# Performance work log

Measured on AMD Instinct MI355X. Metric: run time of the kernel, lower is better.

The kernel has to match this reference:

```python
import jax, jax.numpy as jnp
import numpy as np

N = 50000
E = 800000
IN_C = 128
HID_C = 128
OUT_C = 128
N_CLS = 40


def setup_inputs() -> dict:
    key = jax.random.key(0)
    ks = jax.random.split(key, 12)
    x = jax.random.normal(ks[0], (N, IN_C), dtype=jnp.float32)
    edge_index = jax.random.randint(ks[1], (2, E), 0, N, dtype=jnp.int64)
    s = 1.0 / np.sqrt(IN_C)
    W_l1 = jax.random.uniform(ks[2], (IN_C, HID_C), jnp.float32, -s, s)
    W_r1 = jax.random.uniform(ks[3], (IN_C, HID_C), jnp.float32, -s, s)
    b1 = jax.random.uniform(ks[4], (HID_C,), jnp.float32, -s, s)
    s2 = 1.0 / np.sqrt(HID_C)
    W_l2 = jax.random.uniform(ks[5], (HID_C, OUT_C), jnp.float32, -s2, s2)
    W_r2 = jax.random.uniform(ks[6], (HID_C, OUT_C), jnp.float32, -s2, s2)
    b2 = jax.random.uniform(ks[7], (OUT_C,), jnp.float32, -s2, s2)
    s3 = 1.0 / np.sqrt(OUT_C)
    W_c = jax.random.uniform(ks[8], (OUT_C, N_CLS), jnp.float32, -s3, s3)
    b_c = jax.random.uniform(ks[9], (N_CLS,), jnp.float32, -s3, s3)
    return {"x": x, "edge_index": edge_index, "W_l1": W_l1, "W_r1": W_r1,
            "b1": b1, "W_l2": W_l2, "W_r2": W_r2, "b2": b2,
            "W_c": W_c, "b_c": b_c}


def _mean_aggregate(x, src, dst, deg_inv):
    # gather source node features over edges, scatter-mean to dst nodes
    msg = x[src]  # [E, C]
    agg = jax.ops.segment_sum(msg, dst, num_segments=N)  # [N, C]
    return agg * deg_inv[:, None]


def _sage_conv(x, src, dst, deg_inv, W_l, W_r, b):
    # PyG SAGEConv (mean aggr): out = agg @ W_l + x @ W_r + b
    agg = _mean_aggregate(x, src, dst, deg_inv)
    return agg @ W_l + x @ W_r + b


def reference(x, edge_index, W_l1, W_r1, b1, W_l2, W_r2, b2, W_c, b_c):
    src, dst = edge_index[0], edge_index[1]
    deg = jax.ops.segment_sum(jnp.ones((E,), jnp.float32), dst, num_segments=N)
    deg_inv = jnp.where(deg > 0, 1.0 / jnp.maximum(deg, 1.0), 0.0)
    h = jax.nn.relu(_sage_conv(x, src, dst, deg_inv, W_l1, W_r1, b1))
    h = jax.nn.relu(_sage_conv(h, src, dst, deg_inv, W_l2, W_r2, b2))
    return h @ W_c + b_c
```

## Files before the change

### kernel.cpp

```cpp
#include <hip/hip_runtime.h>

#define N_NODES 50000
#define N_EDGES 800000
#define C 128
#define NCLS 40
#define KB 98
#define BCAP 9216

typedef short bf16x8 __attribute__((ext_vector_type(8)));
typedef float f32x4 __attribute__((ext_vector_type(4)));
typedef unsigned short ushort_t;

__device__ __forceinline__ unsigned short f32_to_bf16(float f) {
    union { float f; unsigned u; } c; c.f = f;
    unsigned r = (c.u + 0x7FFFu + ((c.u >> 16) & 1u)) >> 16;
    return (unsigned short)r;
}
__device__ __forceinline__ float bf_lo(unsigned u) {
    union { unsigned u; float f; } c; c.u = u << 16; return c.f;
}
__device__ __forceinline__ float bf_hi(unsigned u) {
    union { unsigned u; float f; } c; c.u = u & 0xffff0000u; return c.f;
}
__device__ __forceinline__ unsigned pack_bf16(float lo, float hi) {
    return (unsigned)f32_to_bf16(lo) | ((unsigned)f32_to_bf16(hi) << 16);
}

__global__ __launch_bounds__(256)
void convert_all(const float* __restrict__ Wl1, const float* __restrict__ Wr1,
                 const float* __restrict__ Wl2, const float* __restrict__ Wr2,
                 const float* __restrict__ Wc,  const float* __restrict__ x,
                 ushort_t* __restrict__ Wbf1, ushort_t* __restrict__ Wbf2,
                 ushort_t* __restrict__ Wcb,  ushort_t* __restrict__ xb) {
    int b = blockIdx.x;
    int tid = threadIdx.x;
    if (b < 256) {
        const float* Wl = (b < 128) ? Wl1 : Wl2;
        const float* Wr = (b < 128) ? Wr1 : Wr2;
        ushort_t* Bpre  = (b < 128) ? Wbf1 : Wbf2;
        int idx = (b & 127) * 256 + tid;
        int n = idx >> 8;
        int k = idx & 255;
        float v = (k < 128) ? Wl[k * 128 + n] : Wr[(k - 128) * 128 + n];
        Bpre[n * 256 + k] = f32_to_bf16(v);
    } else if (b < 280) {
        int idx = (b - 256) * 256 + tid;
        if (idx < 48 * 128) {
            int n = idx >> 7;
            int k = idx & 127;
            float v = (n < NCLS) ? Wc[k * NCLS + n] : 0.f;
            Wcb[idx] = f32_to_bf16(v);
        }
    } else {
        int idx = (b - 280) * 256 + tid;
        const float4 v0 = *(const float4*)&x[idx * 8];
        const float4 v1 = *(const float4*)&x[idx * 8 + 4];
        uint4 o;
        o.x = pack_bf16(v0.x, v0.y);
        o.y = pack_bf16(v0.z, v0.w);
        o.z = pack_bf16(v1.x, v1.y);
        o.w = pack_bf16(v1.z, v1.w);
        ((uint4*)xb)[idx] = o;
    }
}

__global__ __launch_bounds__(256)
void bin_kernel(const int* __restrict__ src, const int* __restrict__ dst,
                int* __restrict__ bucket_cnt, unsigned* __restrict__ bucket_data) {
    __shared__ int lh[KB];
    int tid = threadIdx.x;
    int e0 = blockIdx.x * 4096;
    if (tid < KB) lh[tid] = 0;
    __syncthreads();
#pragma unroll
    for (int j = 0; j < 16; ++j) {
        int e = e0 + j * 256 + tid;
        if (e < N_EDGES) atomicAdd(&lh[dst[e] >> 9], 1);
    }
    __syncthreads();
    if (tid < KB) lh[tid] = atomicAdd(&bucket_cnt[tid], lh[tid]);
    __syncthreads();
#pragma unroll
    for (int j = 0; j < 16; ++j) {
        int e = e0 + j * 256 + tid;
        if (e < N_EDGES) {
            int d = dst[e];
            int b = d >> 9;
            int pos = atomicAdd(&lh[b], 1);
            if (pos < BCAP)
                bucket_data[b * BCAP + pos] = (unsigned)src[e] | ((unsigned)(d & 511) << 16);
        }
    }
}

__global__ __launch_bounds__(256)
void build_kernel(const int* __restrict__ bucket_cnt, const unsigned* __restrict__ bucket_data,
                  int* __restrict__ row_ptr, ushort_t* __restrict__ csr16,
                  int* __restrict__ perm) {
    __shared__ int wt[4];
    __shared__ int wt2[4];
    __shared__ int sbases[128];
    __shared__ int hist[512];
    __shared__ int loff[512];
    __shared__ int dhist[64];
    __shared__ ushort_t lcsr[BCAP];
    int tid = threadIdx.x;
    int b = blockIdx.x;
    int n0 = b << 9;
    int nb = min(512, N_NODES - n0);

    int v = 0, x = 0;
    if (tid < 128) {
        v = (tid < KB) ? bucket_cnt[tid] : 0;
        x = v;
#pragma unroll
        for (int off = 1; off < 64; off <<= 1) {
            int t = __shfl_up(x, off, 64);
            if ((tid & 63) >= off) x += t;
        }
        if ((tid & 63) == 63) wt[tid >> 6] = x;
    }
    hist[tid] = 0; hist[tid + 256] = 0;
    __syncthreads();
    if (tid < 128) sbases[tid] = x - v + ((tid >= 64) ? wt[0] : 0);
    __syncthreads();
    int base = sbases[b];
    int ecnt = min(bucket_cnt[b], BCAP);

    for (int i = tid; i < ecnt; i += 256)
        atomicAdd(&hist[bucket_data[b * BCAP + i] >> 16], 1);
    __syncthreads();

    int h0 = hist[2 * tid], h1 = hist[2 * tid + 1];
    int s = h0 + h1;
    int y = s;
#pragma unroll
    for (int off = 1; off < 64; off <<= 1) {
        int t = __shfl_up(y, off, 64);
        if ((tid & 63) >= off) y += t;
    }
    if ((tid & 63) == 63) wt2[tid >> 6] = y;
    __syncthreads();
    int add = 0;
    for (int j = 0; j < (tid >> 6); ++j) add += wt2[j];
    int ex = y + add - s;
    loff[2 * tid] = ex;
    loff[2 * tid + 1] = ex + h0;
    __syncthreads();

    for (int n = tid; n < nb; n += 256) row_ptr[n0 + n] = base + loff[n];
    if (b == KB - 1 && tid == 0) row_ptr[N_NODES] = N_EDGES;
    __syncthreads();

    for (int i = tid; i < ecnt; i += 256) {
        unsigned e = bucket_data[b * BCAP + i];
        int pos = atomicAdd(&loff[e >> 16], 1);
        lcsr[pos] = (ushort_t)(e & 0xFFFFu);
    }
    __syncthreads();
    for (int i = tid; i < ecnt; i += 256) csr16[base + i] = lcsr[i];

    if (tid < 64) dhist[tid] = 0;
    for (int p = tid; p < 512; p += 256) perm[(b << 9) + p] = -1;
    __syncthreads();
    int na = 2 * tid, nbb = 2 * tid + 1;
    int c0 = min(h0, 63), c1 = min(h1, 63);
    if (na < nb)  atomicAdd(&dhist[c0], 1);
    if (nbb < nb) atomicAdd(&dhist[c1], 1);
    __syncthreads();
    if (tid < 64) {
        int v2 = dhist[tid];
        int xs = v2;
#pragma unroll
        for (int off = 1; off < 64; off <<= 1) {
            int t = __shfl_up(xs, off, 64);
            if (tid >= off) xs += t;
        }
        dhist[tid] = xs - v2;
    }
    __syncthreads();
    if (na < nb)  { int pos = atomicAdd(&dhist[c0], 1); perm[(b << 9) + pos] = n0 + na; }
    if (nbb < nb) { int pos = atomicAdd(&dhist[c1], 1); perm[(b << 9) + pos] = n0 + nbb; }
}

#define ALD 136
template<int CLS>
__global__ __launch_bounds__(256)
void fused_layer(const ushort_t* __restrict__ feat,
                 const int* __restrict__ row_ptr,
                 const ushort_t* __restrict__ csr16,
                 const int* __restrict__ perm,
                 const ushort_t* __restrict__ Bpre,
                 const float* __restrict__ bias,
                 ushort_t* __restrict__ hout,
                 const ushort_t* __restrict__ Wcb,
                 const float* __restrict__ bc,
                 float* __restrict__ out) {
    __shared__ ushort_t aggL[64 * ALD];
    __shared__ ushort_t stg[64 * 40 + 128 * 40];
    __shared__ int tperm[64];
    ushort_t* AsX = stg;
    ushort_t* BsP = stg + 64 * 40;
    ushort_t* eidx = stg;
    const int tid = threadIdx.x;
    const int r0 = blockIdx.x * 64;
    const int w = tid >> 6, lane = tid & 63, m = lane & 15, quad = lane >> 4;
    const int q = tid & 15;
    const int g = tid >> 4;

    if (tid < 64) tperm[tid] = perm[r0 + tid];
    __syncthreads();

    for (int p = 0; p < 4; ++p) {
        int nl = p * 16 + g;
        int node = tperm[nl];
        int beg = 0, end = 0;
        if (node >= 0) { beg = row_ptr[node]; end = row_ptr[node + 1]; }
        int dl = end - beg; if (dl > 64) dl = 64;
        for (int j = q; j < dl; j += 16) eidx[nl * 64 + j] = csr16[beg + j];
    }
    __syncthreads();

    const uint4* fb = (const uint4*)feat;
    for (int p = 0; p < 4; ++p) {
        int nl = p * 16 + g;
        int node = tperm[nl];
        int beg = 0, end = 0;
        if (node >= 0) { beg = row_ptr[node]; end = row_ptr[node + 1]; }
        int deg = end - beg;
        int dl = deg > 64 ? 64 : deg;
        float a0[8], a1[8], a2[8], a3[8];
#pragma unroll
        for (int j = 0; j < 8; ++j) { a0[j] = 0.f; a1[j] = 0.f; a2[j] = 0.f; a3[j] = 0.f; }
        int i = 0;
        for (; i + 4 <= dl; i += 4) {
            ushort4 s4 = *(const ushort4*)&eidx[nl * 64 + i];
            uint4 v0 = fb[(int)s4.x * 16 + q];
            uint4 v1 = fb[(int)s4.y * 16 + q];
            uint4 v2 = fb[(int)s4.z * 16 + q];
            uint4 v3 = fb[(int)s4.w * 16 + q];
            a0[0] += bf_lo(v0.x); a0[1] += bf_hi(v0.x); a0[2] += bf_lo(v0.y); a0[3] += bf_hi(v0.y);
            a0[4] += bf_lo(v0.z); a0[5] += bf_hi(v0.z); a0[6] += bf_lo(v0.w); a0[7] += bf_hi(v0.w);
            a1[0] += bf_lo(v1.x); a1[1] += bf_hi(v1.x); a1[2] += bf_lo(v1.y); a1[3] += bf_hi(v1.y);
            a1[4] += bf_lo(v1.z); a1[5] += bf_hi(v1.z); a1[6] += bf_lo(v1.w); a1[7] += bf_hi(v1.w);
            a2[0] += bf_lo(v2.x); a2[1] += bf_hi(v2.x); a2[2] += bf_lo(v2.y); a2[3] += bf_hi(v2.y);
            a2[4] += bf_lo(v2.z); a2[5] += bf_hi(v2.z); a2[6] += bf_lo(v2.w); a2[7] += bf_hi(v2.w);
            a3[0] += bf_lo(v3.x); a3[1] += bf_hi(v3.x); a3[2] += bf_lo(v3.y); a3[3] += bf_hi(v3.y);
            a3[4] += bf_lo(v3.z); a3[5] += bf_hi(v3.z); a3[6] += bf_lo(v3.w); a3[7] += bf_hi(v3.w);
        }
        int rem = dl - i;
        if (rem > 0) {
            int s0 = eidx[nl * 64 + i];
            int s1 = eidx[nl * 64 + i + (rem > 1 ? 1 : 0)];
            int s2 = eidx[nl * 64 + i + (rem > 2 ? 2 : 0)];
            uint4 v0 = fb[s0 * 16 + q];
            uint4 v1 = fb[s1 * 16 + q];
            uint4 v2 = fb[s2 * 16 + q];
            float m1 = rem > 1 ? 1.f : 0.f;
            float m2 = rem > 2 ? 1.f : 0.f;
            a0[0] += bf_lo(v0.x); a0[1] += bf_hi(v0.x); a0[2] += bf_lo(v0.y); a0[3] += bf_hi(v0.y);
            a0[4] += bf_lo(v0.z); a0[5] += bf_hi(v0.z); a0[6] += bf_lo(v0.w); a0[7] += bf_hi(v0.w);
            a1[0] += m1 * bf_lo(v1.x); a1[1] += m1 * bf_hi(v1.x); a1[2] += m1 * bf_lo(v1.y); a1[3] += m1 * bf_hi(v1.y);
            a1[4] += m1 * bf_lo(v1.z); a1[5] += m1 * bf_hi(v1.z); a1[6] += m1 * bf_lo(v1.w); a1[7] += m1 * bf_hi(v1.w);
            a2[0] += m2 * bf_lo(v2.x); a2[1] += m2 * bf_hi(v2.x); a2[2] += m2 * bf_lo(v2.y); a2[3] += m2 * bf_hi(v2.y);
            a2[4] += m2 * bf_lo(v2.z); a2[5] += m2 * bf_hi(v2.z); a2[6] += m2 * bf_lo(v2.w); a2[7] += m2 * bf_hi(v2.w);
        }
        for (int j2 = 64; j2 < deg; ++j2) {
            int s0 = csr16[beg + j2];
            uint4 v0 = fb[s0 * 16 + q];
            a0[0] += bf_lo(v0.x); a0[1] += bf_hi(v0.x); a0[2] += bf_lo(v0.y); a0[3] += bf_hi(v0.y);
            a0[4] += bf_lo(v0.z); a0[5] += bf_hi(v0.z); a0[6] += bf_lo(v0.w); a0[7] += bf_hi(v0.w);
        }
        float di = deg > 0 ? 1.f / (float)deg : 0.f;
        float r[8];
#pragma unroll
        for (int j = 0; j < 8; ++j) r[j] = (a0[j] + a1[j] + a2[j] + a3[j]) * di;
        uint4 o;
        o.x = pack_bf16(r[0], r[1]);
        o.y = pack_bf16(r[2], r[3]);
        o.z = pack_bf16(r[4], r[5]);
        o.w = pack_bf16(r[6], r[7]);
        *(uint4*)&aggL[nl * ALD + q * 8] = o;
    }
    __syncthreads();

    f32x4 acc[8];
#pragma unroll
    for (int t = 0; t < 8; ++t) acc[t] = (f32x4){0.f, 0.f, 0.f, 0.f};

    for (int kc = 0; kc < 8; ++kc) {
        if (kc) __syncthreads();
        if (kc >= 4) {
            int row = tid >> 2;
            int kq = tid & 3;
            int nd = tperm[row]; if (nd < 0) nd = 0;
            uint4 v = *(const uint4*)&feat[nd * C + (kc & 3) * 32 + kq * 8];
            *(uint4*)&AsX[row * 40 + kq * 8] = v;
        }
#pragma unroll
        for (int i = 0; i < 2; ++i) {
            int slot = tid + i * 256;
            int n = slot >> 2;
            int qq = slot & 3;
            *(uint4*)&BsP[n * 40 + qq * 8] = *(const uint4*)&Bpre[n * 256 + kc * 32 + qq * 8];
        }
        __syncthreads();
        bf16x8 af = (kc < 4)
            ? *(const bf16x8*)&aggL[(w * 16 + m) * ALD + kc * 32 + quad * 8]
            : *(const bf16x8*)&AsX[(w * 16 + m) * 40 + quad * 8];
#pragma unroll
        for (int t = 0; t < 8; ++t) {
            bf16x8 bf = *(const bf16x8*)&BsP[(t * 16 + m) * 40 + quad * 8];
            acc[t] = __builtin_amdgcn_mfma_f32_16x16x32_bf16(af, bf, acc[t], 0, 0, 0);
        }
    }

    int prow[4];
#pragma unroll
    for (int reg = 0; reg < 4; ++reg) prow[reg] = tperm[w * 16 + quad * 4 + reg];

    if (CLS == 0) {
#pragma unroll
        for (int t = 0; t < 8; ++t) {
            int colv = t * 16 + m;
            float bv = bias[colv];
#pragma unroll
            for (int reg = 0; reg < 4; ++reg) {
                int rg = prow[reg];
                if (rg >= 0) {
                    float vv = fmaxf(acc[t][reg] + bv, 0.f);
                    hout[rg * C + colv] = f32_to_bf16(vv);
                }
            }
        }
    } else {
        __syncthreads();
#pragma unroll
        for (int t = 0; t < 8; ++t) {
            int colv = t * 16 + m;
            float bv = bias[colv];
#pragma unroll
            for (int reg = 0; reg < 4; ++reg) {
                int rl = w * 16 + quad * 4 + reg;
                float vv = fmaxf(acc[t][reg] + bv, 0.f);
                aggL[rl * ALD + colv] = f32_to_bf16(vv);
            }
        }
#pragma unroll
        for (int i = 0; i < 3; ++i) {
            int slot = tid + i * 256;
            int n = slot >> 4, kq = slot & 15;
            uint4 vv = *(const uint4*)&Wcb[n * C + kq * 8];
            *(uint4*)&stg[(kq >> 2) * (48 * 40) + n * 40 + (kq & 3) * 8] = vv;
        }
        __syncthreads();
        f32x4 acc2[3];
#pragma unroll
        for (int t = 0; t < 3; ++t) acc2[t] = (f32x4){0.f, 0.f, 0.f, 0.f};
#pragma unroll
        for (int kc = 0; kc < 4; ++kc) {
            bf16x8 af = *(const bf16x8*)&aggL[(w * 16 + m) * ALD + kc * 32 + quad * 8];
#pragma unroll
            for (int t = 0; t < 3; ++t) {
                bf16x8 bf = *(const bf16x8*)&stg[kc * (48 * 40) + (t * 16 + m) * 40 + quad * 8];
                acc2[t] = __builtin_amdgcn_mfma_f32_16x16x32_bf16(af, bf, acc2[t], 0, 0, 0);
            }
        }
#pragma unroll
        for (int t = 0; t < 3; ++t) {
            int col = t * 16 + m;
            if (col < NCLS) {
                float bvv = bc[col];
#pragma unroll
                for (int reg = 0; reg < 4; ++reg) {
                    int rg = prow[reg];
                    if (rg >= 0) out[rg * NCLS + col] = acc2[t][reg] + bvv;
                }
            }
        }
    }
}

extern "C" void kernel_launch(void* const* d_in, const int* in_sizes, int n_in,
                              void* d_out, int out_size, void* d_ws, size_t ws_size,
                              hipStream_t stream) {
    const float* x   = (const float*)d_in[0];
    const int*   ei  = (const int*)d_in[1];
    const float* Wl1 = (const float*)d_in[2];
    const float* Wr1 = (const float*)d_in[3];
    const float* b1  = (const float*)d_in[4];
    const float* Wl2 = (const float*)d_in[5];
    const float* Wr2 = (const float*)d_in[6];
    const float* b2  = (const float*)d_in[7];
    const float* Wc  = (const float*)d_in[8];
    const float* bc  = (const float*)d_in[9];
    const int* srcI = ei;
    const int* dstI = ei + N_EDGES;
    float* out = (float*)d_out;

    ushort_t* xb   = (ushort_t*)d_ws;
    ushort_t* h1b  = xb + (size_t)N_NODES * C;
    ushort_t* Wbf1 = h1b + (size_t)N_NODES * C;
    ushort_t* Wbf2 = Wbf1 + 32768;
    ushort_t* Wcb  = Wbf2 + 32768;
    ushort_t* csr16 = Wcb + 6144;
    int* bucket_cnt = (int*)(csr16 + N_EDGES);
    int* row_ptr    = bucket_cnt + 128;
    unsigned* bucket_data = (unsigned*)(row_ptr + N_NODES + 1);
    int* perm = (int*)(bucket_data + (size_t)KB * BCAP);

    convert_all<<<280 + (N_NODES * C / 8 + 255) / 256, 256, 0, stream>>>(
        Wl1, Wr1, Wl2, Wr2, Wc, x, Wbf1, Wbf2, Wcb, xb);

    hipMemsetAsync(bucket_cnt, 0, 128 * sizeof(int), stream);
    bin_kernel<<<(N_EDGES + 4095) / 4096, 256, 0, stream>>>(srcI, dstI, bucket_cnt, bucket_data);
    build_kernel<<<KB, 256, 0, stream>>>(bucket_cnt, bucket_data, row_ptr, csr16, perm);

    fused_layer<0><<<KB * 8, 256, 0, stream>>>(
        xb, row_ptr, csr16, perm, Wbf1, b1, h1b, nullptr, nullptr, nullptr);

    fused_layer<1><<<KB * 8, 256, 0, stream>>>(
        h1b, row_ptr, csr16, perm, Wbf2, b2, nullptr, Wcb, bc, out);
}
```

Measured before the change: 216.8 us.

## Split fused gather+GEMM layer into separate gather and dense GEMM kernels

Each layer's fused aggregate-then-GEMM kernel is unfused into a gather kernel and a GEMM kernel. The gather kernel handles 16 nodes per block, reads edge indices straight from global memory with one-step software prefetch, and writes the mean-aggregated features to a new workspace buffer. The GEMM kernel then tiles contiguous rows in natural order and no longer needs the perm indirection. This aims to cut per-block imbalance and LDS/sync overhead in the fused kernel. In exchange it adds an extra round trip of the aggregated features through global memory and two more kernel launches.

New measurement: 224.0 us. +3.3%, slower.

```diff
diff --git a/kernel.cpp b/kernel.cpp
--- a/kernel.cpp
+++ b/kernel.cpp
@@ -183,106 +183,98 @@
     if (nbb < nb) { int pos = atomicAdd(&dhist[c1], 1); perm[(b << 9) + pos] = n0 + nbb; }
 }
 
+__global__ __launch_bounds__(256)
+void gather_kernel(const ushort_t* __restrict__ feat,
+                   const int* __restrict__ row_ptr,
+                   const ushort_t* __restrict__ csr16,
+                   const int* __restrict__ perm,
+                   ushort_t* __restrict__ agg) {
+    const int tid = threadIdx.x;
+    const int q = tid & 15;
+    const int g = tid >> 4;
+    int slot = blockIdx.x * 16 + g;
+    int node = perm[slot];
+    if (node < 0) return;
+    int beg = row_ptr[node], end = row_ptr[node + 1];
+    int deg = end - beg;
+    const uint4* fb = (const uint4*)feat;
+
+    float a0[8], a1[8], a2[8], a3[8];
+#pragma unroll
+    for (int j = 0; j < 8; ++j) { a0[j] = 0.f; a1[j] = 0.f; a2[j] = 0.f; a3[j] = 0.f; }
+
+    int nquad = deg >> 2;
+    int sx0 = 0, sx1 = 0, sx2 = 0, sx3 = 0;
+    if (nquad > 0) {
+        sx0 = csr16[beg]; sx1 = csr16[beg + 1]; sx2 = csr16[beg + 2]; sx3 = csr16[beg + 3];
+    }
+    for (int qd = 0; qd < nquad; ++qd) {
+        int s0 = sx0, s1 = sx1, s2 = sx2, s3 = sx3;
+        uint4 v0 = fb[s0 * 16 + q];
+        uint4 v1 = fb[s1 * 16 + q];
+        uint4 v2 = fb[s2 * 16 + q];
+        uint4 v3 = fb[s3 * 16 + q];
+        if (qd + 1 < nquad) {
+            int bs = beg + (qd + 1) * 4;
+            sx0 = csr16[bs]; sx1 = csr16[bs + 1]; sx2 = csr16[bs + 2]; sx3 = csr16[bs + 3];
+        }
+        a0[0] += bf_lo(v0.x); a0[1] += bf_hi(v0.x); a0[2] += bf_lo(v0.y); a0[3] += bf_hi(v0.y);
+        a0[4] += bf_lo(v0.z); a0[5] += bf_hi(v0.z); a0[6] += bf_lo(v0.w); a0[7] += bf_hi(v0.w);
+        a1[0] += bf_lo(v1.x); a1[1] += bf_hi(v1.x); a1[2] += bf_lo(v1.y); a1[3] += bf_hi(v1.y);
+        a1[4] += bf_lo(v1.z); a1[5] += bf_hi(v1.z); a1[6] += bf_lo(v1.w); a1[7] += bf_hi(v1.w);
+        a2[0] += bf_lo(v2.x); a2[1] += bf_hi(v2.x); a2[2] += bf_lo(v2.y); a2[3] += bf_hi(v2.y);
+        a2[4] += bf_lo(v2.z); a2[5] += bf_hi(v2.z); a2[6] += bf_lo(v2.w); a2[7] += bf_hi(v2.w);
+        a3[0] += bf_lo(v3.x); a3[1] += bf_hi(v3.x); a3[2] += bf_lo(v3.y); a3[3] += bf_hi(v3.y);
+        a3[4] += bf_lo(v3.z); a3[5] += bf_hi(v3.z); a3[6] += bf_lo(v3.w); a3[7] += bf_hi(v3.w);
+    }
+    int i0 = beg + nquad * 4;
+    int rem = end - i0;
+    if (rem > 0) {
+        int s0 = csr16[i0];
+        int s1 = csr16[i0 + (rem > 1 ? 1 : 0)];
+        int s2 = csr16[i0 + (rem > 2 ? 2 : 0)];
+        uint4 v0 = fb[s0 * 16 + q];
+        uint4 v1 = fb[s1 * 16 + q];
+        uint4 v2 = fb[s2 * 16 + q];
+        float m1 = rem > 1 ? 1.f : 0.f;
+        float m2 = rem > 2 ? 1.f : 0.f;
+        a0[0] += bf_lo(v0.x); a0[1] += bf_hi(v0.x); a0[2] += bf_lo(v0.y); a0[3] += bf_hi(v0.y);
+        a0[4] += bf_lo(v0.z); a0[5] += bf_hi(v0.z); a0[6] += bf_lo(v0.w); a0[7] += bf_hi(v0.w);
+        a1[0] += m1 * bf_lo(v1.x); a1[1] += m1 * bf_hi(v1.x); a1[2] += m1 * bf_lo(v1.y); a1[3] += m1 * bf_hi(v1.y);
+        a1[4] += m1 * bf_lo(v1.z); a1[5] += m1 * bf_hi(v1.z); a1[6] += m1 * bf_lo(v1.w); a1[7] += m1 * bf_hi(v1.w);
+        a2[0] += m2 * bf_lo(v2.x); a2[1] += m2 * bf_hi(v2.x); a2[2] += m2 * bf_lo(v2.y); a2[3] += m2 * bf_hi(v2.y);
+        a2[4] += m2 * bf_lo(v2.z); a2[5] += m2 * bf_hi(v2.z); a2[6] += m2 * bf_lo(v2.w); a2[7] += m2 * bf_hi(v2.w);
+    }
+    float di = deg > 0 ? 1.f / (float)deg : 0.f;
+    float r[8];
+#pragma unroll
+    for (int j = 0; j < 8; ++j) r[j] = (a0[j] + a1[j] + a2[j] + a3[j]) * di;
+    uint4 o;
+    o.x = pack_bf16(r[0], r[1]);
+    o.y = pack_bf16(r[2], r[3]);
+    o.z = pack_bf16(r[4], r[5]);
+    o.w = pack_bf16(r[6], r[7]);
+    *(uint4*)&agg[node * C + q * 8] = o;
+}
+
 #define ALD 136
 template<int CLS>
 __global__ __launch_bounds__(256)
-void fused_layer(const ushort_t* __restrict__ feat,
-                 const int* __restrict__ row_ptr,
-                 const ushort_t* __restrict__ csr16,
-                 const int* __restrict__ perm,
-                 const ushort_t* __restrict__ Bpre,
-                 const float* __restrict__ bias,
-                 ushort_t* __restrict__ hout,
-                 const ushort_t* __restrict__ Wcb,
-                 const float* __restrict__ bc,
-                 float* __restrict__ out) {
-    __shared__ ushort_t aggL[64 * ALD];
+void gemm_layer(const ushort_t* __restrict__ agg,
+                const ushort_t* __restrict__ feat,
+                const ushort_t* __restrict__ Bpre,
+                const float* __restrict__ bias,
+                ushort_t* __restrict__ hout,
+                const ushort_t* __restrict__ Wcb,
+                const float* __restrict__ bc,
+                float* __restrict__ out) {
     __shared__ ushort_t stg[64 * 40 + 128 * 40];
-    __shared__ int tperm[64];
-    ushort_t* AsX = stg;
-    ushort_t* BsP = stg + 64 * 40;
-    ushort_t* eidx = stg;
+    __shared__ ushort_t h2L[CLS ? 64 * ALD : 4];
+    ushort_t* As = stg;
+    ushort_t* Bs = stg + 64 * 40;
     const int tid = threadIdx.x;
     const int r0 = blockIdx.x * 64;
     const int w = tid >> 6, lane = tid & 63, m = lane & 15, quad = lane >> 4;
-    const int q = tid & 15;
-    const int g = tid >> 4;
-
-    if (tid < 64) tperm[tid] = perm[r0 + tid];
-    __syncthreads();
-
-    for (int p = 0; p < 4; ++p) {
-        int nl = p * 16 + g;
-        int node = tperm[nl];
-        int beg = 0, end = 0;
-        if (node >= 0) { beg = row_ptr[node]; end = row_ptr[node + 1]; }
-        int dl = end - beg; if (dl > 64) dl = 64;
-        for (int j = q; j < dl; j += 16) eidx[nl * 64 + j] = csr16[beg + j];
-    }
-    __syncthreads();
-
-    const uint4* fb = (const uint4*)feat;
-    for (int p = 0; p < 4; ++p) {
-        int nl = p * 16 + g;
-        int node = tperm[nl];
-        int beg = 0, end = 0;
-        if (node >= 0) { beg = row_ptr[node]; end = row_ptr[node + 1]; }
-        int deg = end - beg;
-        int dl = deg > 64 ? 64 : deg;
-        float a0[8], a1[8], a2[8], a3[8];
-#pragma unroll
-        for (int j = 0; j < 8; ++j) { a0[j] = 0.f; a1[j] = 0.f; a2[j] = 0.f; a3[j] = 0.f; }
-        int i = 0;
-        for (; i + 4 <= dl; i += 4) {
-            ushort4 s4 = *(const ushort4*)&eidx[nl * 64 + i];
-            uint4 v0 = fb[(int)s4.x * 16 + q];
-            uint4 v1 = fb[(int)s4.y * 16 + q];
-            uint4 v2 = fb[(int)s4.z * 16 + q];
-            uint4 v3 = fb[(int)s4.w * 16 + q];
-            a0[0] += bf_lo(v0.x); a0[1] += bf_hi(v0.x); a0[2] += bf_lo(v0.y); a0[3] += bf_hi(v0.y);
-            a0[4] += bf_lo(v0.z); a0[5] += bf_hi(v0.z); a0[6] += bf_lo(v0.w); a0[7] += bf_hi(v0.w);
-            a1[0] += bf_lo(v1.x); a1[1] += bf_hi(v1.x); a1[2] += bf_lo(v1.y); a1[3] += bf_hi(v1.y);
-            a1[4] += bf_lo(v1.z); a1[5] += bf_hi(v1.z); a1[6] += bf_lo(v1.w); a1[7] += bf_hi(v1.w);
-            a2[0] += bf_lo(v2.x); a2[1] += bf_hi(v2.x); a2[2] += bf_lo(v2.y); a2[3] += bf_hi(v2.y);
-            a2[4] += bf_lo(v2.z); a2[5] += bf_hi(v2.z); a2[6] += bf_lo(v2.w); a2[7] += bf_hi(v2.w);
-            a3[0] += bf_lo(v3.x); a3[1] += bf_hi(v3.x); a3[2] += bf_lo(v3.y); a3[3] += bf_hi(v3.y);
-            a3[4] += bf_lo(v3.z); a3[5] += bf_hi(v3.z); a3[6] += bf_lo(v3.w); a3[7] += bf_hi(v3.w);
-        }
-        int rem = dl - i;
-        if (rem > 0) {
-            int s0 = eidx[nl * 64 + i];
-            int s1 = eidx[nl * 64 + i + (rem > 1 ? 1 : 0)];
-            int s2 = eidx[nl * 64 + i + (rem > 2 ? 2 : 0)];
-            uint4 v0 = fb[s0 * 16 + q];
-            uint4 v1 = fb[s1 * 16 + q];
-            uint4 v2 = fb[s2 * 16 + q];
-            float m1 = rem > 1 ? 1.f : 0.f;
-            float m2 = rem > 2 ? 1.f : 0.f;
-            a0[0] += bf_lo(v0.x); a0[1] += bf_hi(v0.x); a0[2] += bf_lo(v0.y); a0[3] += bf_hi(v0.y);
-            a0[4] += bf_lo(v0.z); a0[5] += bf_hi(v0.z); a0[6] += bf_lo(v0.w); a0[7] += bf_hi(v0.w);
-            a1[0] += m1 * bf_lo(v1.x); a1[1] += m1 * bf_hi(v1.x); a1[2] += m1 * bf_lo(v1.y); a1[3] += m1 * bf_hi(v1.y);
-            a1[4] += m1 * bf_lo(v1.z); a1[5] += m1 * bf_hi(v1.z); a1[6] += m1 * bf_lo(v1.w); a1[7] += m1 * bf_hi(v1.w);
-            a2[0] += m2 * bf_lo(v2.x); a2[1] += m2 * bf_hi(v2.x); a2[2] += m2 * bf_lo(v2.y); a2[3] += m2 * bf_hi(v2.y);
-            a2[4] += m2 * bf_lo(v2.z); a2[5] += m2 * bf_hi(v2.z); a2[6] += m2 * bf_lo(v2.w); a2[7] += m2 * bf_hi(v2.w);
-        }
-        for (int j2 = 64; j2 < deg; ++j2) {
-            int s0 = csr16[beg + j2];
-            uint4 v0 = fb[s0 * 16 + q];
-            a0[0] += bf_lo(v0.x); a0[1] += bf_hi(v0.x); a0[2] += bf_lo(v0.y); a0[3] += bf_hi(v0.y);
-            a0[4] += bf_lo(v0.z); a0[5] += bf_hi(v0.z); a0[6] += bf_lo(v0.w); a0[7] += bf_hi(v0.w);
-        }
-        float di = deg > 0 ? 1.f / (float)deg : 0.f;
-        float r[8];
-#pragma unroll
-        for (int j = 0; j < 8; ++j) r[j] = (a0[j] + a1[j] + a2[j] + a3[j]) * di;
-        uint4 o;
-        o.x = pack_bf16(r[0], r[1]);
-        o.y = pack_bf16(r[2], r[3]);
-        o.z = pack_bf16(r[4], r[5]);
-        o.w = pack_bf16(r[6], r[7]);
-        *(uint4*)&aggL[nl * ALD + q * 8] = o;
-    }
-    __syncthreads();
 
     f32x4 acc[8];
 #pragma unroll
@@ -290,34 +282,29 @@
 
     for (int kc = 0; kc < 8; ++kc) {
         if (kc) __syncthreads();
-        if (kc >= 4) {
+        {
             int row = tid >> 2;
             int kq = tid & 3;
-            int nd = tperm[row]; if (nd < 0) nd = 0;
-            uint4 v = *(const uint4*)&feat[nd * C + (kc & 3) * 32 + kq * 8];
-            *(uint4*)&AsX[row * 40 + kq * 8] = v;
+            int rg = r0 + row; if (rg >= N_NODES) rg = N_NODES - 1;
+            const ushort_t* srcp = (kc < 4) ? agg : feat;
+            uint4 v = *(const uint4*)&srcp[rg * C + (kc & 3) * 32 + kq * 8];
+            *(uint4*)&As[row * 40 + kq * 8] = v;
         }
 #pragma unroll
         for (int i = 0; i < 2; ++i) {
             int slot = tid + i * 256;
             int n = slot >> 2;
             int qq = slot & 3;
-            *(uint4*)&BsP[n * 40 + qq * 8] = *(const uint4*)&Bpre[n * 256 + kc * 32 + qq * 8];
+            *(uint4*)&Bs[n * 40 + qq * 8] = *(const uint4*)&Bpre[n * 256 + kc * 32 + qq * 8];
         }
         __syncthreads();
-        bf16x8 af = (kc < 4)
-            ? *(const bf16x8*)&aggL[(w * 16 + m) * ALD + kc * 32 + quad * 8]
-            : *(const bf16x8*)&AsX[(w * 16 + m) * 40 + quad * 8];
+        bf16x8 af = *(const bf16x8*)&As[(w * 16 + m) * 40 + quad * 8];
 #pragma unroll
         for (int t = 0; t < 8; ++t) {
-            bf16x8 bf = *(const bf16x8*)&BsP[(t * 16 + m) * 40 + quad * 8];
+            bf16x8 bf = *(const bf16x8*)&Bs[(t * 16 + m) * 40 + quad * 8];
             acc[t] = __builtin_amdgcn_mfma_f32_16x16x32_bf16(af, bf, acc[t], 0, 0, 0);
         }
     }
-
-    int prow[4];
-#pragma unroll
-    for (int reg = 0; reg < 4; ++reg) prow[reg] = tperm[w * 16 + quad * 4 + reg];
 
     if (CLS == 0) {
 #pragma unroll
@@ -326,8 +313,8 @@
             float bv = bias[colv];
 #pragma unroll
             for (int reg = 0; reg < 4; ++reg) {
-                int rg = prow[reg];
-                if (rg >= 0) {
+                int rg = r0 + w * 16 + quad * 4 + reg;
+                if (rg < N_NODES) {
                     float vv = fmaxf(acc[t][reg] + bv, 0.f);
                     hout[rg * C + colv] = f32_to_bf16(vv);
                 }
@@ -343,7 +330,7 @@
             for (int reg = 0; reg < 4; ++reg) {
                 int rl = w * 16 + quad * 4 + reg;
                 float vv = fmaxf(acc[t][reg] + bv, 0.f);
-                aggL[rl * ALD + colv] = f32_to_bf16(vv);
+                h2L[rl * ALD + colv] = f32_to_bf16(vv);
             }
         }
 #pragma unroll
@@ -359,7 +346,7 @@
         for (int t = 0; t < 3; ++t) acc2[t] = (f32x4){0.f, 0.f, 0.f, 0.f};
 #pragma unroll
         for (int kc = 0; kc < 4; ++kc) {
-            bf16x8 af = *(const bf16x8*)&aggL[(w * 16 + m) * ALD + kc * 32 + quad * 8];
+            bf16x8 af = *(const bf16x8*)&h2L[(w * 16 + m) * ALD + kc * 32 + quad * 8];
 #pragma unroll
             for (int t = 0; t < 3; ++t) {
                 bf16x8 bf = *(const bf16x8*)&stg[kc * (48 * 40) + (t * 16 + m) * 40 + quad * 8];
@@ -373,8 +360,8 @@
                 float bvv = bc[col];
 #pragma unroll
                 for (int reg = 0; reg < 4; ++reg) {
-                    int rg = prow[reg];
-                    if (rg >= 0) out[rg * NCLS + col] = acc2[t][reg] + bvv;
+                    int rg = r0 + w * 16 + quad * 4 + reg;
+                    if (rg < N_NODES) out[rg * NCLS + col] = acc2[t][reg] + bvv;
                 }
             }
         }
@@ -408,6 +395,7 @@
     int* row_ptr    = bucket_cnt + 128;
     unsigned* bucket_data = (unsigned*)(row_ptr + N_NODES + 1);
     int* perm = (int*)(bucket_data + (size_t)KB * BCAP);
+    ushort_t* aggb = (ushort_t*)(perm + KB * 512);
 
     convert_all<<<280 + (N_NODES * C / 8 + 255) / 256, 256, 0, stream>>>(
         Wl1, Wr1, Wl2, Wr2, Wc, x, Wbf1, Wbf2, Wcb, xb);
@@ -416,9 +404,11 @@
     bin_kernel<<<(N_EDGES + 4095) / 4096, 256, 0, stream>>>(srcI, dstI, bucket_cnt, bucket_data);
     build_kernel<<<KB, 256, 0, stream>>>(bucket_cnt, bucket_data, row_ptr, csr16, perm);
 
-    fused_layer<0><<<KB * 8, 256, 0, stream>>>(
-        xb, row_ptr, csr16, perm, Wbf1, b1, h1b, nullptr, nullptr, nullptr);
-
-    fused_layer<1><<<KB * 8, 256, 0, stream>>>(
-        h1b, row_ptr, csr16, perm, Wbf2, b2, nullptr, Wcb, bc, out);
-}
+    gather_kernel<<<KB * 512 / 16, 256, 0, stream>>>(xb, row_ptr, csr16, perm, aggb);
+    gemm_layer<0><<<(N_NODES + 63) / 64, 256, 0, stream>>>(
+        aggb, xb, Wbf1, b1, h1b, nullptr, nullptr, nullptr);
+
+    gather_kernel<<<KB * 512 / 16, 256, 0, stream>>>(h1b, row_ptr, csr16, perm, aggb);
+    gemm_layer<1><<<(N_NODES + 63) / 64, 256, 0, stream>>>(
+        aggb, h1b, Wbf2, b2, nullptr, Wcb, bc, out);
+}
```
